# Kernel optimization log

Measured on AMD Instinct MI355X. Metric: run time of the kernel, lower is better.

The kernel has to match this reference:

```python
import jax, jax.numpy as jnp
import numpy as np

COST_CLASS = 1.0
COST_POINT = 1.0


def _linear_sum_assignment(cost):
    """Pure-numpy Jonker-Volgenant / Hungarian (e-maxx formulation).
    Emulates scipy.optimize.linear_sum_assignment for a dense float cost matrix.
    Returns (row_ind, col_ind) with row_ind sorted ascending.
    """
    cost = np.asarray(cost, dtype=np.float64)
    transposed = cost.shape[0] > cost.shape[1]
    if transposed:
        cost = cost.T
    n, m = cost.shape  # n <= m
    INF = np.inf
    u = np.zeros(n + 1)
    v = np.zeros(m + 1)
    p = np.zeros(m + 1, dtype=np.int64)  # p[j] = row (1-indexed) matched to col j
    for i in range(1, n + 1):
        p[0] = i
        j0 = 0
        minv = np.full(m + 1, INF)
        way = np.zeros(m + 1, dtype=np.int64)
        used = np.zeros(m + 1, dtype=bool)
        while True:
            used[j0] = True
            i0 = p[j0]
            cur = cost[i0 - 1, :] - u[i0] - v[1:]
            free = ~used[1:]
            upd = free & (cur < minv[1:])
            minv[1:][upd] = cur[upd]
            way[1:][upd] = j0
            masked = np.where(free, minv[1:], INF)
            j1 = int(np.argmin(masked)) + 1
            delta = masked[j1 - 1]
            u[p[used]] += delta
            v[used] -= delta
            minv[1:][free] -= delta
            j0 = j1
            if p[j0] == 0:
                break
        while j0 != 0:
            j1 = way[j0]
            p[j0] = p[j1]
            j0 = j1
    ans = np.zeros(n, dtype=np.int64)  # ans[row] = col
    for j in range(1, m + 1):
        if p[j] > 0:
            ans[p[j] - 1] = j - 1
    if transposed:
        # rows of the original matrix are ans values; sort by original row index
        order = np.argsort(ans)
        return ans[order], np.arange(n, dtype=np.int64)[order]
    return np.arange(n, dtype=np.int64), ans


def _cost_matrix(pred_logits, pred_points, tgt_labels, tgt_points):
    bs, Q, C = pred_logits.shape
    T = tgt_labels.shape[1]
    out_prob = jax.nn.softmax(pred_logits.reshape(bs * Q, C), axis=-1)   # [bs*Q, C]
    out_points = pred_points.reshape(bs * Q, -1)                          # [bs*Q, 2]
    tgt_ids = tgt_labels.reshape(-1)                                      # [bs*T]
    tgt_pts = tgt_points.reshape(bs * T, -1).astype(jnp.float32)          # [bs*T, 2]
    cost_class = -out_prob[:, tgt_ids]                                    # [bs*Q, bs*T]
    # L1 cdist
    cost_point = jnp.sum(jnp.abs(out_points[:, None, :] - tgt_pts[None, :, :]), axis=-1)
    Cfull = COST_POINT * cost_point + COST_CLASS * cost_class             # [bs*Q, bs*T]
    # per-batch diagonal blocks (what the scipy split selects): [bs, Q, T]
    C4 = Cfull.reshape(bs, Q, bs, T)
    Cb = C4[jnp.arange(bs), :, jnp.arange(bs), :]
    return Cb


def setup_inputs() -> dict:
    key = jax.random.key(0)
    k1, k2, k3, k4 = jax.random.split(key, 4)
    bs, Q, C, T = 16, 1024, 92, 128
    return {
        "pred_logits": jax.random.normal(k1, (bs, Q, C), dtype=jnp.float32),
        "pred_points": jax.random.uniform(k2, (bs, Q, 2), dtype=jnp.float32),
        "tgt_labels": jax.random.randint(k3, (bs, T), 0, C, dtype=jnp.int64),
        "tgt_points": jax.random.uniform(k4, (bs, T, 2), dtype=jnp.float32),
    }


def reference(pred_logits, pred_points, tgt_labels, tgt_points):
    Cb = _cost_matrix(pred_logits, pred_points, tgt_labels, tgt_points)   # [bs, Q, T]
    Cnp = np.asarray(jax.device_get(Cb))
    rows, cols = [], []
    for b in range(Cnp.shape[0]):  # structural loop over batch for the assignment
        r, c = _linear_sum_assignment(Cnp[b])
        rows.append(r)
        cols.append(c)
    row_idx = jnp.asarray(np.stack(rows))  # [bs, T] selected query indices (sorted)
    col_idx = jnp.asarray(np.stack(cols))  # [bs, T] matched target indices
    return Cb, row_idx, col_idx
```

## Files before the change

### kernel.cpp

```cpp
#include <hip/hip_runtime.h>
#include <hip/hip_bf16.h>
#include <math.h>

#define BS 16
#define Q 1024
#define CC 92
#define T 128
#define M 1024
#define NR 128
#define NQB 16

__global__ __launch_bounds__(256) void prep_kernel(
    const float* __restrict__ logits,
    const float* __restrict__ ppts,
    const int*   __restrict__ tlab,
    const float* __restrict__ tpts,
    float* __restrict__ Cb,
    float* __restrict__ CbT,
    unsigned long long* __restrict__ part)
{
    const int blk = blockIdx.x;
    const int b   = blk >> 4;
    const int qb  = blk & 15;
    const int q0  = qb * 64;
    const int tid = threadIdx.x;
    const int lane = tid & 63;

    __shared__ float lg[64 * CC];
    __shared__ float tile[128][68];
    __shared__ float tx_sh[T], ty_sh[T];
    __shared__ int   lab_sh[T];
    __shared__ float mx_sh[64], inv_sh[64], px_sh[64], py_sh[64];

    if (tid < T) {
        lab_sh[tid] = tlab[b * T + tid];
        tx_sh[tid]  = tpts[(b * T + tid) * 2 + 0];
        ty_sh[tid]  = tpts[(b * T + tid) * 2 + 1];
    }
    if (tid < 64) {
        px_sh[tid] = ppts[((size_t)b * Q + q0 + tid) * 2 + 0];
        py_sh[tid] = ppts[((size_t)b * Q + q0 + tid) * 2 + 1];
    }
    const float* lbase = logits + ((size_t)b * Q + q0) * CC;
    for (int idx = tid; idx < 64 * CC; idx += 256) lg[idx] = lbase[idx];
    __syncthreads();

    {
        const int w = tid >> 6;
        for (int s = 0; s < 16; ++s) {
            const int ql = w * 16 + s;
            const float* c = &lg[ql * CC];
            float l0 = c[lane];
            float l1 = (lane + 64 < CC) ? c[lane + 64] : -INFINITY;
            float mx = fmaxf(l0, l1);
            #pragma unroll
            for (int off = 32; off > 0; off >>= 1)
                mx = fmaxf(mx, __shfl_down(mx, off));
            mx = __shfl(mx, 0);
            float es = expf(l0 - mx) + ((lane + 64 < CC) ? expf(l1 - mx) : 0.0f);
            #pragma unroll
            for (int off = 32; off > 0; off >>= 1) es += __shfl_down(es, off);
            es = __shfl(es, 0);
            if (lane == 0) { mx_sh[ql] = mx; inv_sh[ql] = 1.0f / es; }
        }
    }
    __syncthreads();

    {
        const int ql = tid >> 2;
        const int tc = tid & 3;
        const float px = px_sh[ql], py = py_sh[ql];
        const float mx = mx_sh[ql], inv = inv_sh[ql];
        const float* lgq = &lg[ql * CC];
        float* cbrow = Cb + ((size_t)b * Q + q0 + ql) * T + tc * 32;
        #pragma unroll
        for (int k = 0; k < 8; ++k) {
            float4 o;
            #pragma unroll
            for (int e = 0; e < 4; ++e) {
                const int t = tc * 32 + 4 * k + e;
                const int labv = lab_sh[t];
                float prob = expf(lgq[labv] - mx) * inv;
                float cp   = fabsf(px - tx_sh[t]) + fabsf(py - ty_sh[t]);
                float val  = cp - prob;
                (&o.x)[e] = val;
                tile[t][ql] = val;
            }
            ((float4*)cbrow)[k] = o;
        }
    }
    __syncthreads();

    {
        const int rg = tid >> 4;
        const int c4 = tid & 15;
        #pragma unroll
        for (int it = 0; it < 8; ++it) {
            const int t = it * 16 + rg;
            float4 v = *(const float4*)&tile[t][4 * c4];
            *(float4*)(CbT + ((size_t)b * NR + t) * Q + q0 + 4 * c4) = v;

            unsigned long long bk = ~0ull;
            const float* vf = (const float*)&v;
            #pragma unroll
            for (int e = 0; e < 4; ++e) {
                unsigned bits = __float_as_uint(vf[e]);
                unsigned mono = (bits & 0x80000000u) ? ~bits
                                                     : (bits | 0x80000000u);
                const int j = q0 + 4 * c4 + e;
                unsigned long long key =
                    ((unsigned long long)mono << 10) | (unsigned)j;
                bk = (key < bk) ? key : bk;
            }
            #pragma unroll
            for (int off = 1; off < 16; off <<= 1) {
                unsigned long long ok = __shfl_xor(bk, off);
                bk = (ok < bk) ? ok : bk;
            }
            if (c4 == 0) part[((size_t)b * NQB + qb) * NR + t] = bk;
        }
    }
}

__global__ __launch_bounds__(256) void cost_kernel(
    const float* __restrict__ logits, const float* __restrict__ ppts,
    const int* __restrict__ tlab, const float* __restrict__ tpts,
    float* __restrict__ Cb)
{
    const int blk  = blockIdx.x;
    const int b    = blk >> 8;
    const int wave = threadIdx.x >> 6;
    const int lane = threadIdx.x & 63;
    const int q    = (blk & 255) * 4 + wave;

    __shared__ float tx_sh[T], ty_sh[T];
    __shared__ int   lab_sh[T];
    __shared__ float logit_sh[4][CC];

    if (threadIdx.x < T) {
        lab_sh[threadIdx.x] = tlab[b * T + threadIdx.x];
        tx_sh[threadIdx.x]  = tpts[(b * T + threadIdx.x) * 2 + 0];
        ty_sh[threadIdx.x]  = tpts[(b * T + threadIdx.x) * 2 + 1];
    }
    const float* lrow = logits + ((size_t)b * Q + q) * CC;
    float l0 = lrow[lane];
    float l1 = (lane + 64 < CC) ? lrow[lane + 64] : -INFINITY;
    logit_sh[wave][lane] = l0;
    if (lane + 64 < CC) logit_sh[wave][lane + 64] = l1;

    float mx = fmaxf(l0, l1);
    #pragma unroll
    for (int off = 32; off > 0; off >>= 1) mx = fmaxf(mx, __shfl_down(mx, off));
    mx = __shfl(mx, 0);
    float es = expf(l0 - mx) + ((lane + 64 < CC) ? expf(l1 - mx) : 0.0f);
    #pragma unroll
    for (int off = 32; off > 0; off >>= 1) es += __shfl_down(es, off);
    es = __shfl(es, 0);
    const float inv = 1.0f / es;
    const float px = ppts[((size_t)b * Q + q) * 2 + 0];
    const float py = ppts[((size_t)b * Q + q) * 2 + 1];
    __syncthreads();
    float* outrow = Cb + ((size_t)b * Q + q) * T;
    #pragma unroll
    for (int t = lane; t < T; t += 64) {
        int   labv = lab_sh[t];
        float prob = expf(logit_sh[wave][labv] - mx) * inv;
        float cp   = fabsf(px - tx_sh[t]) + fabsf(py - ty_sh[t]);
        outrow[t]  = cp - prob;
    }
}

#define DPP_UMIN_STEP(x, ctrl)                                              \
    {                                                                       \
        unsigned _t = (unsigned)__builtin_amdgcn_update_dpp(                \
            (int)(x), (int)(x), (ctrl), 0xF, 0xF, false);                   \
        (x) = ((x) < _t) ? (x) : _t;                                        \
    }

template<int USET>
__global__ __launch_bounds__(64) void solve_kernel(
    const float* __restrict__ Cb,
    const float* __restrict__ CbT,
    const unsigned long long* __restrict__ part,
    float* __restrict__ out_rows,
    float* __restrict__ out_cols)
{
    const int b    = blockIdx.x;
    const int lane = threadIdx.x;

    __shared__ int    row4col[M];
    __shared__ int    col4row[NR];
    __shared__ float  u_sh[NR];
    __shared__ int    path_lds[M];
    __shared__ int    SRr[NR];
    __shared__ float  SRd[NR];
    __shared__ int    minj_sh[NR];
    __shared__ int    claim[M];

    const float* CbB  = Cb  + (size_t)b * Q * T;
    const float* CbTB = CbT + (size_t)b * NR * Q;

    for (int j = lane; j < M;  j += 64) { row4col[j] = -1; claim[j] = 0x7fffffff; }
    for (int i = lane; i < NR; i += 64) col4row[i] = -1;

    if (part) {
        #pragma unroll
        for (int r2 = 0; r2 < 2; ++r2) {
            const int r = lane + 64 * r2;
            const unsigned long long* pr = part + (size_t)b * NQB * NR + r;
            unsigned long long k = pr[0];
            #pragma unroll
            for (int i = 1; i < NQB; ++i) {
                unsigned long long o = pr[(size_t)i * NR];
                k = (o < k) ? o : k;
            }
            minj_sh[r] = (int)(k & 1023u);
            unsigned mono = (unsigned)(k >> 10);
            unsigned bits = (mono & 0x80000000u) ? (mono ^ 0x80000000u) : ~mono;
            u_sh[r] = __uint_as_float(bits);
        }
    } else {
        for (int i = lane; i < NR; i += 64) { minj_sh[i] = -1; u_sh[i] = 0.0f; }
    }
    __syncthreads();

    if (part) {
        #pragma unroll
        for (int r2 = 0; r2 < 2; ++r2) {
            const int r = lane + 64 * r2;
            atomicMin(&claim[minj_sh[r]], r);
        }
        __syncthreads();
        #pragma unroll
        for (int r2 = 0; r2 < 2; ++r2) {
            const int r = lane + 64 * r2;
            const int mj = minj_sh[r];
            if (claim[mj] == r) { col4row[r] = mj; row4col[mj] = r; }
        }
        __syncthreads();
    }

    unsigned long long um0 = ~__ballot(col4row[lane] >= 0);
    unsigned long long um1 = ~__ballot(col4row[lane + 64] >= 0);

    const float FINF = INFINITY;
    float v_[16], dist_[16];
    #pragma unroll
    for (int k = 0; k < 16; ++k) v_[k] = 0.0f;

    for (int half = 0; half < 2; ++half) {
        unsigned long long mask = half ? um1 : um0;
        while (mask) {
            const int curRow = __ffsll(mask) - 1 + 64 * half;
            mask &= mask - 1;

            #pragma unroll
            for (int k = 0; k < 16; ++k) dist_[k] = FINF;
            unsigned used  = 0;
            float    minVal = 0.0f;
            int      i_s  = curRow;
            int      sink = -1;
            int      cnt  = 0;

            for (int guard = 0; guard <= M; ++guard) {
                const float ui = u_sh[i_s];
                const float s  = minVal - ui;

                float4 c4[4];
                if (USET) {
                    const float4* row = (const float4*)(CbTB + (size_t)i_s * Q);
                    #pragma unroll
                    for (int g = 0; g < 4; ++g) c4[g] = row[lane + 64 * g];
                } else {
                    const float* col = CbB + i_s;
                    #pragma unroll
                    for (int g = 0; g < 4; ++g) {
                        float* cf = (float*)&c4[g];
                        #pragma unroll
                        for (int e = 0; e < 4; ++e)
                            cf[e] = col[(size_t)(256 * g + 4 * lane + e) * T];
                    }
                }

                float lmin = FINF; int lidx = 0;
                #pragma unroll
                for (int g = 0; g < 4; ++g) {
                    const float* cf = (const float*)&c4[g];
                    #pragma unroll
                    for (int e = 0; e < 4; ++e) {
                        const int k = 4 * g + e;
                        const int j = 256 * g + 4 * lane + e;
                        const bool fr = ((used >> k) & 1u) == 0u;
                        float r = s + cf[e] - v_[k];
                        if (fr && r < dist_[k]) {
                            dist_[k] = r;
                            path_lds[256 * g + 64 * e + lane] = i_s;
                        }
                        float a = fr ? dist_[k] : FINF;
                        if (a < lmin) { lmin = a; lidx = j; }
                    }
                }

                const int cand = row4col[lidx];

                unsigned bits  = __float_as_uint(lmin);
                unsigned lmono = (bits & 0x80000000u) ? ~bits
                                                      : (bits | 0x80000000u);

                unsigned rmin = lmono;
                DPP_UMIN_STEP(rmin, 0x111);
                DPP_UMIN_STEP(rmin, 0x112);
                DPP_UMIN_STEP(rmin, 0x114);
                DPP_UMIN_STEP(rmin, 0x118);
                DPP_UMIN_STEP(rmin, 0x142);
                DPP_UMIN_STEP(rmin, 0x143);
                const unsigned gmin =
                    (unsigned)__builtin_amdgcn_readlane((int)rmin, 63);

                const unsigned long long bmask = __ballot(lmono == gmin);
                const int winner = __ffsll(bmask) - 1;

                minVal = __uint_as_float(
                    (unsigned)__builtin_amdgcn_readlane(
                        (int)__float_as_uint(lmin), winner));
                const int jstar = __builtin_amdgcn_readlane(lidx, winner);

                if (((jstar >> 2) & 63) == lane)
                    used |= (1u << (((jstar >> 8) << 2) | (jstar & 3)));

                const int ra = __builtin_amdgcn_readlane(cand, winner);
                if (ra == -1) { sink = jstar; break; }
                if (lane == 0 && cnt < NR) { SRr[cnt] = ra; SRd[cnt] = minVal; }
                cnt++;
                i_s = ra;
            }

            #pragma unroll
            for (int k = 0; k < 16; ++k)
                if ((used >> k) & 1u) v_[k] += dist_[k] - minVal;

            if (lane == 0) u_sh[curRow] += minVal;
            for (int t = lane; t < cnt; t += 64)
                u_sh[SRr[t]] += minVal - SRd[t];

            if (lane == 0) {
                int j = sink;
                for (int g2 = 0; g2 < NR + 2; ++g2) {
                    int pi = path_lds[((j >> 8) << 8) | ((j & 3) << 6) |
                                      ((j >> 2) & 63)];
                    row4col[j] = pi;
                    int jn = col4row[pi];
                    col4row[pi] = j;
                    if (pi == curRow) break;
                    j = jn;
                }
            }
            __syncthreads();
        }
    }

    int base = 0;
    #pragma unroll
    for (int g = 0; g < 4; ++g) {
        int tv[4], mt[4];
        #pragma unroll
        for (int e = 0; e < 4; ++e) {
            const int j = 256 * g + 4 * lane + e;
            tv[e] = row4col[j];
            mt[e] = (tv[e] >= 0);
        }
        unsigned long long B[4];
        #pragma unroll
        for (int e = 0; e < 4; ++e) B[e] = __ballot(mt[e] != 0);
        const unsigned long long low = (1ull << lane) - 1ull;
        int below = base;
        #pragma unroll
        for (int e = 0; e < 4; ++e) below += __popcll(B[e] & low);
        int local = 0;
        #pragma unroll
        for (int e = 0; e < 4; ++e) {
            if (mt[e]) {
                const int rank = below + local;
                const int j = 256 * g + 4 * lane + e;
                out_rows[b * NR + rank] = (float)j;
                out_cols[b * NR + rank] = (float)tv[e];
                ++local;
            }
        }
        #pragma unroll
        for (int e = 0; e < 4; ++e) base += __popcll(B[e]);
    }
}

extern "C" void kernel_launch(void* const* d_in, const int* in_sizes, int n_in,
                              void* d_out, int out_size, void* d_ws, size_t ws_size,
                              hipStream_t stream) {
    const float* logits = (const float*)d_in[0];
    const float* ppts   = (const float*)d_in[1];
    const int*   tlab   = (const int*)  d_in[2];
    const float* tpts   = (const float*)d_in[3];

    float* Cb   = (float*)d_out;
    float* rows = Cb + (size_t)BS * Q * T;
    float* cols = rows + (size_t)BS * T;

    float* CbT = (float*)d_ws;
    unsigned long long* part =
        (unsigned long long*)((char*)d_ws + (size_t)BS * NR * Q * sizeof(float));

    const size_t need = (size_t)BS * NR * Q * sizeof(float)
                      + (size_t)BS * NQB * NR * sizeof(unsigned long long);

    if (ws_size >= need) {
        prep_kernel<<<BS * NQB, 256, 0, stream>>>(logits, ppts, tlab, tpts,
                                                  Cb, CbT, part);
        solve_kernel<1><<<BS, 64, 0, stream>>>(Cb, CbT, part, rows, cols);
    } else {
        cost_kernel<<<4096, 256, 0, stream>>>(logits, ppts, tlab, tpts, Cb);
        solve_kernel<0><<<BS, 64, 0, stream>>>(Cb, CbT, nullptr, rows, cols);
    }
}
```

Baseline: 131.0 us.

## Add auction-style augmenting row reduction before shortest-path phase in solver

Adds an augmenting row reduction pass (as in LAPJV) that, for each unassigned row, finds its best and second-best reduced cost and greedily assigns or displaces rows, adjusting u and v, for up to 48 steps. This aims to assign most rows cheaply before the costlier Dijkstra-style shortest augmenting path loop. It also swaps the block-index mapping in the prep kernel so neighbouring blocks cover different batches. The greedy phase adds extra reductions per step and, in the worst case, can cycle without improving the assignment.

```diff
diff --git a/kernel.cpp b/kernel.cpp
--- a/kernel.cpp
+++ b/kernel.cpp
@@ -20,8 +20,8 @@
     unsigned long long* __restrict__ part)
 {
     const int blk = blockIdx.x;
-    const int b   = blk >> 4;
-    const int qb  = blk & 15;
+    const int b   = blk & 15;
+    const int qb  = blk >> 4;
     const int q0  = qb * 64;
     const int tid = threadIdx.x;
     const int lane = tid & 63;
@@ -177,6 +177,20 @@
         (x) = ((x) < _t) ? (x) : _t;                                        \
     }
 
+#define DPP_UMIN_REDUCE(x)                                                  \
+    DPP_UMIN_STEP(x, 0x111); DPP_UMIN_STEP(x, 0x112);                       \
+    DPP_UMIN_STEP(x, 0x114); DPP_UMIN_STEP(x, 0x118);                       \
+    DPP_UMIN_STEP(x, 0x142); DPP_UMIN_STEP(x, 0x143);
+
+__device__ __forceinline__ unsigned mono_enc(float f) {
+    unsigned b = __float_as_uint(f);
+    return (b & 0x80000000u) ? ~b : (b | 0x80000000u);
+}
+__device__ __forceinline__ float mono_dec(unsigned m) {
+    unsigned b = (m & 0x80000000u) ? (m ^ 0x80000000u) : ~m;
+    return __uint_as_float(b);
+}
+
 template<int USET>
 __global__ __launch_bounds__(64) void solve_kernel(
     const float* __restrict__ Cb,
@@ -215,9 +229,7 @@
                 k = (o < k) ? o : k;
             }
             minj_sh[r] = (int)(k & 1023u);
-            unsigned mono = (unsigned)(k >> 10);
-            unsigned bits = (mono & 0x80000000u) ? (mono ^ 0x80000000u) : ~mono;
-            u_sh[r] = __uint_as_float(bits);
+            u_sh[r] = mono_dec((unsigned)(k >> 10));
         }
     } else {
         for (int i = lane; i < NR; i += 64) { minj_sh[i] = -1; u_sh[i] = 0.0f; }
@@ -240,13 +252,90 @@
         __syncthreads();
     }
 
-    unsigned long long um0 = ~__ballot(col4row[lane] >= 0);
-    unsigned long long um1 = ~__ballot(col4row[lane + 64] >= 0);
-
     const float FINF = INFINITY;
     float v_[16], dist_[16];
     #pragma unroll
     for (int k = 0; k < 16; ++k) v_[k] = 0.0f;
+
+    {
+        unsigned long long am0 = ~__ballot(col4row[lane] >= 0);
+        unsigned long long am1 = ~__ballot(col4row[lane + 64] >= 0);
+        for (int half = 0; half < 2; ++half) {
+            unsigned long long mask = half ? am1 : am0;
+            while (mask) {
+                int cur = __ffsll(mask) - 1 + 64 * half;
+                mask &= mask - 1;
+
+                for (int step = 0; step < 48; ++step) {
+                    const float ucur = u_sh[cur];
+
+                    float4 c4[4];
+                    if (USET) {
+                        const float4* row =
+                            (const float4*)(CbTB + (size_t)cur * Q);
+                        #pragma unroll
+                        for (int g = 0; g < 4; ++g) c4[g] = row[lane + 64 * g];
+                    } else {
+                        const float* col = CbB + cur;
+                        #pragma unroll
+                        for (int g = 0; g < 4; ++g) {
+                            float* cf = (float*)&c4[g];
+                            #pragma unroll
+                            for (int e = 0; e < 4; ++e)
+                                cf[e] = col[(size_t)(256*g + 4*lane + e) * T];
+                        }
+                    }
+
+                    float m1l = FINF, m2l = FINF; int j1l = 0;
+                    #pragma unroll
+                    for (int g = 0; g < 4; ++g) {
+                        const float* cf = (const float*)&c4[g];
+                        #pragma unroll
+                        for (int e = 0; e < 4; ++e) {
+                            const int k = 4 * g + e;
+                            const int j = 256 * g + 4 * lane + e;
+                            float r = cf[e] - ucur - v_[k];
+                            if (r < m1l) { m2l = m1l; m1l = r; j1l = j; }
+                            else if (r < m2l) { m2l = r; }
+                        }
+                    }
+
+                    unsigned e1 = mono_enc(m1l);
+                    unsigned r1 = e1;
+                    DPP_UMIN_REDUCE(r1);
+                    const unsigned g1 =
+                        (unsigned)__builtin_amdgcn_readlane((int)r1, 63);
+                    const unsigned long long bm = __ballot(e1 == g1);
+                    const int winner = __ffsll(bm) - 1;
+                    const int j1 = __builtin_amdgcn_readlane(j1l, winner);
+                    const float m1 = mono_dec(g1);
+
+                    unsigned e2 = mono_enc((lane == winner) ? m2l : m1l);
+                    DPP_UMIN_REDUCE(e2);
+                    const float m2 = mono_dec(
+                        (unsigned)__builtin_amdgcn_readlane((int)e2, 63));
+
+                    if (lane == 0) u_sh[cur] = ucur + m2;
+                    if (((j1 >> 2) & 63) == lane) {
+                        const int k = ((j1 >> 8) << 2) | (j1 & 3);
+                        v_[k] -= (m2 - m1);
+                    }
+
+                    const int disp = row4col[j1];
+                    if (lane == 0) {
+                        row4col[j1]  = cur;
+                        col4row[cur] = j1;
+                        if (disp >= 0) col4row[disp] = -1;
+                    }
+                    if (disp < 0) { cur = -1; break; }
+                    cur = disp;
+                }
+            }
+        }
+    }
+
+    unsigned long long um0 = ~__ballot(col4row[lane] >= 0);
+    unsigned long long um1 = ~__ballot(col4row[lane + 64] >= 0);
 
     for (int half = 0; half < 2; ++half) {
         unsigned long long mask = half ? um1 : um0;
@@ -303,17 +392,9 @@
 
                 const int cand = row4col[lidx];
 
-                unsigned bits  = __float_as_uint(lmin);
-                unsigned lmono = (bits & 0x80000000u) ? ~bits
-                                                      : (bits | 0x80000000u);
-
+                unsigned lmono = mono_enc(lmin);
                 unsigned rmin = lmono;
-                DPP_UMIN_STEP(rmin, 0x111);
-                DPP_UMIN_STEP(rmin, 0x112);
-                DPP_UMIN_STEP(rmin, 0x114);
-                DPP_UMIN_STEP(rmin, 0x118);
-                DPP_UMIN_STEP(rmin, 0x142);
-                DPP_UMIN_STEP(rmin, 0x143);
+                DPP_UMIN_REDUCE(rmin);
                 const unsigned gmin =
                     (unsigned)__builtin_amdgcn_readlane((int)rmin, 63);
 
```

New measurement: 127.7 us. 2.5% less time.
